# Kernel tuning notes

Hardware: AMD Instinct MI355X
Metric: run time of the kernel (lower is better)

Reference implementation:

```python
import jax, jax.numpy as jnp
import numpy as np

N = 50000      # nodes
F = 128        # in_channels
H = 4          # heads
C = 32         # out_channels per head
E = 800000     # edges (before self-loops)
NEG_SLOPE = 0.2


def setup_inputs() -> dict:
    key = jax.random.key(0)
    ks = jax.random.split(key, 10)
    x = jax.random.normal(ks[0], (N, F), dtype=jnp.float32)
    edge_index = jax.random.randint(ks[1], (2, E), 0, N, dtype=jnp.int32)
    s = 1.0 / np.sqrt(F)
    Wl = jax.random.uniform(ks[2], (H * C, F), jnp.float32, -s, s)
    bl = jax.random.uniform(ks[3], (H * C,), jnp.float32, -s, s)
    Wr = jax.random.uniform(ks[4], (H * C, F), jnp.float32, -s, s)
    br = jax.random.uniform(ks[5], (H * C,), jnp.float32, -s, s)
    Ws = jax.random.uniform(ks[6], (H * C, F), jnp.float32, -s, s)
    bs = jax.random.uniform(ks[7], (H * C,), jnp.float32, -s, s)
    att = jax.random.normal(ks[8], (H, C), jnp.float32) * (1.0 / np.sqrt(C))
    bias = jnp.zeros((H * C,), jnp.float32)
    return {"x": x, "edge_index": edge_index, "Wl": Wl, "bl": bl,
            "Wr": Wr, "br": br, "Ws": Ws, "bs": bs, "att": att, "bias": bias}


def reference(x, edge_index, Wl, bl, Wr, br, Ws, bs, att, bias):
    # add self loops (add_self_loops=True, edge_dim=None)
    loop = jnp.arange(N, dtype=edge_index.dtype)
    src = jnp.concatenate([edge_index[0], loop])  # j (source / neighbor)
    dst = jnp.concatenate([edge_index[1], loop])  # i (target, softmax segment)

    xl = (x @ Wl.T + bl).reshape(N, H, C)  # attention source transform (lin_l = lin_lAP)
    xr = (x @ Wr.T + br).reshape(N, H, C)  # attention target transform (lin_r = lin_rAP)
    xs = (x @ Ws.T + bs).reshape(N, H, C)  # aggregation transform (lin_s, linAggrSharing=False)

    # GATv2 edge score: a^T LeakyReLU(Theta_l x_j + Theta_r x_i)
    e = jax.nn.leaky_relu(xl[src] + xr[dst], NEG_SLOPE)      # [E+N, H, C]
    score = jnp.einsum('ehc,hc->eh', e, att)                 # [E+N, H]

    # segment softmax over incoming edges of each target node
    m = jax.ops.segment_max(score, dst, num_segments=N)      # [N, H]
    p = jnp.exp(score - m[dst])
    denom = jax.ops.segment_sum(p, dst, num_segments=N)      # [N, H]
    alpha = p / denom[dst]                                   # [E+N, H]

    # weighted scatter-add aggregation of lin_s-transformed sources
    out = jax.ops.segment_sum(xs[src] * alpha[..., None], dst, num_segments=N)
    return out.reshape(N, H * C) + bias                      # concat=True
```

## Files before the change

### kernel.cpp

```cpp
#include <hip/hip_runtime.h>
#include <hip/hip_bf16.h>

#define GN 50000
#define GF 128
#define GH 4
#define GC 32
#define GE 800000
#define GETOT (GE + GN)
#define HC 128
#define NEG 0.2f

#define TBLK ((GN + 63) / 64)
#define SBLK ((GETOT + 255) / 256)

typedef __bf16 bf16x8 __attribute__((ext_vector_type(8)));
typedef float  f32x4  __attribute__((ext_vector_type(4)));
typedef unsigned short ushort8 __attribute__((ext_vector_type(8)));

__device__ __forceinline__ ushort f32_to_bf16_rne(float f) {
    unsigned u = __float_as_uint(f);
    return (ushort)((u + 0x7fffu + ((u >> 16) & 1u)) >> 16);
}

__device__ __forceinline__ bf16x8 cvt8(const float* p) {
    float4 v0 = *(const float4*)p;
    float4 v1 = *(const float4*)(p + 4);
    ushort8 o;
    o[0] = f32_to_bf16_rne(v0.x); o[1] = f32_to_bf16_rne(v0.y);
    o[2] = f32_to_bf16_rne(v0.z); o[3] = f32_to_bf16_rne(v0.w);
    o[4] = f32_to_bf16_rne(v1.x); o[5] = f32_to_bf16_rne(v1.y);
    o[6] = f32_to_bf16_rne(v1.z); o[7] = f32_to_bf16_rne(v1.w);
    return __builtin_bit_cast(bf16x8, o);
}

template<int CTRL>
__device__ __forceinline__ float dpp_add(float v) {
    int s = __builtin_bit_cast(int, v);
    int y = __builtin_amdgcn_update_dpp(s, s, CTRL, 0xF, 0xF, false);
    return v + __builtin_bit_cast(float, y);
}

__global__ __launch_bounds__(256) void conv_w(
    const float* __restrict__ Wl, const float* __restrict__ Wr,
    const float* __restrict__ Ws, ushort* __restrict__ Wb,
    int* __restrict__ deg)
{
    int idx = blockIdx.x * 256 + threadIdx.x;
    if (idx < 3 * GF * GF / 8) {
        int m = idx / 2048;
        int e = (idx - m * 2048) * 8;
        const float* W = (m == 0) ? Wl : (m == 1) ? Wr : Ws;
        float4 v0 = *(const float4*)&W[e];
        float4 v1 = *(const float4*)&W[e + 4];
        ushort8 o;
        o[0] = f32_to_bf16_rne(v0.x); o[1] = f32_to_bf16_rne(v0.y);
        o[2] = f32_to_bf16_rne(v0.z); o[3] = f32_to_bf16_rne(v0.w);
        o[4] = f32_to_bf16_rne(v1.x); o[5] = f32_to_bf16_rne(v1.y);
        o[6] = f32_to_bf16_rne(v1.z); o[7] = f32_to_bf16_rne(v1.w);
        *(ushort8*)&Wb[m * 16384 + e] = o;
    }
    int z = idx - 6144;
    if (z >= 0 && z < GN / 4)
        *(int4*)&deg[z * 4] = make_int4(0, 0, 0, 0);
}

__global__ __launch_bounds__(256) void fused_transform_slot(
    const float* __restrict__ x, const ushort* __restrict__ Wb,
    const float* __restrict__ bl, const float* __restrict__ br,
    const float* __restrict__ bs,
    const int* __restrict__ ei, int* __restrict__ deg, int* __restrict__ slot,
    ushort* __restrict__ xi, float* __restrict__ xr)
{
    if (blockIdx.x < SBLK) {
        int e = blockIdx.x * 256 + threadIdx.x;
        if (e < GETOT) {
            int dst = (e < GE) ? ei[GE + e] : (e - GE);
            slot[e] = atomicAdd(&deg[dst], 1);
        }
        return;
    }

    const int bx    = blockIdx.x - SBLK;
    const int wave  = threadIdx.x >> 6;
    const int lane  = threadIdx.x & 63;
    const int colb  = lane & 15;
    const int klane = lane >> 4;
    const int row0  = bx * 64 + wave * 16;

    bf16x8 a[4];
    {
        int rA = row0 + colb;
        const float* ap = x + (size_t)min(rA, GN - 1) * GF + klane * 8;
#pragma unroll
        for (int kb = 0; kb < 4; ++kb)
            a[kb] = cvt8(ap + kb * 32);
    }

    for (int m = 0; m < 3; ++m) {
        const ushort* wb = Wb + m * 16384 + colb * GF + klane * 8;

        f32x4 acc[8];
#pragma unroll
        for (int n = 0; n < 8; ++n) acc[n] = (f32x4){0.f, 0.f, 0.f, 0.f};

#pragma unroll
        for (int kb = 0; kb < 4; ++kb) {
            bf16x8 b[8];
#pragma unroll
            for (int n = 0; n < 8; ++n)
                b[n] = *(const bf16x8*)(wb + n * 2048 + kb * 32);
#pragma unroll
            for (int n = 0; n < 8; ++n)
                acc[n] = __builtin_amdgcn_mfma_f32_16x16x32_bf16(a[kb], b[n], acc[n], 0, 0, 0);
        }

        const float* bia = (m == 0) ? bl : (m == 1) ? br : bs;
        const int moff = (m == 2) ? 2 : 0;
        const int rD0 = row0 + klane * 4;
#pragma unroll
        for (int n = 0; n < 8; ++n) {
            int col = n * 16 + colb;
            float bv = bia[col];
#pragma unroll
            for (int r = 0; r < 4; ++r) {
                int row = rD0 + r;
                if (row < GN) {
                    float v = acc[n][r] + bv;
                    if (m == 1)
                        xr[(size_t)row * HC + col] = v;
                    else
                        xi[(size_t)row * 256 + (col >> 1) * 4 + (col & 1) + moff]
                            = f32_to_bf16_rne(v);
                }
            }
        }
    }
}

__global__ __launch_bounds__(1024) void scan_kernel(const int* __restrict__ deg,
                                                    int* __restrict__ rowstart)
{
    __shared__ int sums[1024];
    const int t = threadIdx.x;
    const int CH = 52;
    const int start = t * CH;
    const int end = min(start + CH, GN);

    int s = 0;
    if (start + CH <= GN) {
#pragma unroll
        for (int g = 0; g < 13; ++g) {
            int4 v = *(const int4*)&deg[start + g * 4];
            s += v.x + v.y + v.z + v.w;
        }
    } else {
        for (int i = start; i < end; ++i) s += deg[i];
    }
    sums[t] = s;
    __syncthreads();
    for (int off = 1; off < 1024; off <<= 1) {
        int v = (t >= off) ? sums[t - off] : 0;
        __syncthreads();
        sums[t] += v;
        __syncthreads();
    }
    int run = sums[t] - s;
    if (start + CH <= GN) {
#pragma unroll
        for (int g = 0; g < 13; ++g) {
            int4 v = *(const int4*)&deg[start + g * 4];
            int4 w;
            w.x = run;
            w.y = run + v.x;
            w.z = run + v.x + v.y;
            w.w = run + v.x + v.y + v.z;
            run += v.x + v.y + v.z + v.w;
            *(int4*)&rowstart[start + g * 4] = w;
        }
    } else {
        for (int i = start; i < end; ++i) { rowstart[i] = run; run += deg[i]; }
    }
    if (t == 1023) rowstart[GN] = run;
}

__global__ void scatter_kernel(const int* __restrict__ ei,
                               const int* __restrict__ rowstart,
                               const int* __restrict__ slot,
                               int* __restrict__ csr_src)
{
    int e = blockIdx.x * 256 + threadIdx.x;
    if (e >= GETOT) return;
    int src, dst;
    if (e < GE) { src = ei[e]; dst = ei[GE + e]; }
    else        { src = dst = e - GE; }
    csr_src[rowstart[dst] + slot[e]] = src;
}

__device__ __forceinline__ void edge_acc(uint2 xv, float2 xr2, float2 at2,
                                         bool live, float& denom,
                                         float& ax, float& ay)
{
    float zx = __uint_as_float((xv.x & 0xffffu) << 16) + xr2.x;
    float zy = __uint_as_float(xv.x & 0xffff0000u) + xr2.y;
    zx = (zx > 0.f) ? zx : NEG * zx;
    zy = (zy > 0.f) ? zy : NEG * zy;
    float sc = fmaf(zx, at2.x, zy * at2.y);
    sc = dpp_add<0xB1>(sc);
    sc = dpp_add<0x4E>(sc);
    sc = dpp_add<0x124>(sc);
    sc = dpp_add<0x128>(sc);
    float pe = live ? __expf(sc) : 0.f;
    denom += pe;
    ax = fmaf(pe, __uint_as_float((xv.y & 0xffffu) << 16), ax);
    ay = fmaf(pe, __uint_as_float(xv.y & 0xffff0000u), ay);
}

__global__ __launch_bounds__(256) void gat_kernel(
    const ushort* __restrict__ xi, const float* __restrict__ xr,
    const float* __restrict__ att, const float* __restrict__ bias,
    const int* __restrict__ rowstart, const int* __restrict__ csr_src,
    float* __restrict__ out)
{
    const int wave = threadIdx.x >> 6;
    const int lane = threadIdx.x & 63;
    const int node = blockIdx.x * 4 + wave;
    const int l4 = lane * 4;

    const float2 xr2 = *(const float2*)&xr[(size_t)node * HC + lane * 2];
    const float2 at2 = *(const float2*)&att[lane * 2];
    const float2 bi2 = *(const float2*)&bias[lane * 2];

    const int s0 = rowstart[node];
    const int s1 = rowstart[node + 1];

    float denom = 0.f, ax = 0.f, ay = 0.f;
    for (int base = s0; base < s1; base += 64) {
        int nsrc = (base + lane < s1) ? csr_src[base + lane] : 0;
        int cnt = min(64, s1 - base);
        for (int t = 0; t < cnt; t += 4) {
            int sA = __shfl(nsrc, t, 64);
            int sB = __shfl(nsrc, t + 1, 64);
            int sC = __shfl(nsrc, t + 2, 64);
            int sD = __shfl(nsrc, t + 3, 64);
            uint2 vA = *(const uint2*)&xi[(size_t)sA * 256 + l4];
            uint2 vB = *(const uint2*)&xi[(size_t)sB * 256 + l4];
            uint2 vC = *(const uint2*)&xi[(size_t)sC * 256 + l4];
            uint2 vD = *(const uint2*)&xi[(size_t)sD * 256 + l4];
            edge_acc(vA, xr2, at2, true,          denom, ax, ay);
            edge_acc(vB, xr2, at2, (t + 1 < cnt), denom, ax, ay);
            edge_acc(vC, xr2, at2, (t + 2 < cnt), denom, ax, ay);
            edge_acc(vD, xr2, at2, (t + 3 < cnt), denom, ax, ay);
        }
    }
    const float inv = 1.f / denom;
    float2 o;
    o.x = fmaf(ax, inv, bi2.x);
    o.y = fmaf(ay, inv, bi2.y);
    *(float2*)&out[(size_t)node * HC + lane * 2] = o;
}

extern "C" void kernel_launch(void* const* d_in, const int* in_sizes, int n_in,
                              void* d_out, int out_size, void* d_ws, size_t ws_size,
                              hipStream_t stream)
{
    const float* x   = (const float*)d_in[0];
    const int*   ei  = (const int*)  d_in[1];
    const float* Wl  = (const float*)d_in[2];
    const float* bl  = (const float*)d_in[3];
    const float* Wr  = (const float*)d_in[4];
    const float* br  = (const float*)d_in[5];
    const float* Ws  = (const float*)d_in[6];
    const float* bs  = (const float*)d_in[7];
    const float* att = (const float*)d_in[8];
    const float* bias= (const float*)d_in[9];
    float* out = (float*)d_out;

    ushort* xi = (ushort*)d_ws;
    ushort* Wb = xi + (size_t)GN * 256;
    float*  xr = (float*)(Wb + 3 * GF * GF);
    int* deg      = (int*)(xr + (size_t)GN * HC);
    int* rowstart = deg + GN;
    int* slot     = rowstart + GN + 1;
    int* csr_src  = slot + GETOT;

    conv_w<<<(6144 + GN / 4 + 255) / 256, 256, 0, stream>>>(Wl, Wr, Ws, Wb, deg);

    fused_transform_slot<<<SBLK + TBLK, 256, 0, stream>>>(
        x, Wb, bl, br, bs, ei, deg, slot, xi, xr);

    scan_kernel<<<1, 1024, 0, stream>>>(deg, rowstart);

    scatter_kernel<<<SBLK, 256, 0, stream>>>(ei, rowstart, slot, csr_src);

    gat_kernel<<<GN / 4, 256, 0, stream>>>((const ushort*)xi, xr, att, bias,
                                           rowstart, csr_src, out);
}
```

Measured before the change: 285.9 us.

## Stage transform outputs through LDS for coalesced stores and pack xl/xs interleaved

The transform kernel now computes the Wl and Ws products together, packs their bf16 results pairwise into 32-bit words and stages them through shared memory, so each row is written with coalesced 16-byte stores. The xr output goes through the same LDS staging. The packed xi layout shrinks from 256 ushorts to 128 uints per row, and the gather kernel's unpacking is adjusted to match. Block order is also swapped so the transform blocks come before the slot-counting blocks. This aims to cut uncoalesced scattered 2-byte and 4-byte global stores, at the cost of about 33KB of LDS per block, which may lower occupancy.

Result: faster. 248.7 us (-13.0%).

```diff
diff --git a/kernel.cpp b/kernel.cpp
--- a/kernel.cpp
+++ b/kernel.cpp
@@ -12,24 +12,25 @@
 
 #define TBLK ((GN + 63) / 64)
 #define SBLK ((GETOT + 255) / 256)
+#define LDSW 132
 
 typedef __bf16 bf16x8 __attribute__((ext_vector_type(8)));
 typedef float  f32x4  __attribute__((ext_vector_type(4)));
 typedef unsigned short ushort8 __attribute__((ext_vector_type(8)));
 
-__device__ __forceinline__ ushort f32_to_bf16_rne(float f) {
+__device__ __forceinline__ uint f32_to_bf16_rne(float f) {
     unsigned u = __float_as_uint(f);
-    return (ushort)((u + 0x7fffu + ((u >> 16) & 1u)) >> 16);
+    return (u + 0x7fffu + ((u >> 16) & 1u)) >> 16;
 }
 
 __device__ __forceinline__ bf16x8 cvt8(const float* p) {
     float4 v0 = *(const float4*)p;
     float4 v1 = *(const float4*)(p + 4);
     ushort8 o;
-    o[0] = f32_to_bf16_rne(v0.x); o[1] = f32_to_bf16_rne(v0.y);
-    o[2] = f32_to_bf16_rne(v0.z); o[3] = f32_to_bf16_rne(v0.w);
-    o[4] = f32_to_bf16_rne(v1.x); o[5] = f32_to_bf16_rne(v1.y);
-    o[6] = f32_to_bf16_rne(v1.z); o[7] = f32_to_bf16_rne(v1.w);
+    o[0] = (ushort)f32_to_bf16_rne(v0.x); o[1] = (ushort)f32_to_bf16_rne(v0.y);
+    o[2] = (ushort)f32_to_bf16_rne(v0.z); o[3] = (ushort)f32_to_bf16_rne(v0.w);
+    o[4] = (ushort)f32_to_bf16_rne(v1.x); o[5] = (ushort)f32_to_bf16_rne(v1.y);
+    o[6] = (ushort)f32_to_bf16_rne(v1.z); o[7] = (ushort)f32_to_bf16_rne(v1.w);
     return __builtin_bit_cast(bf16x8, o);
 }
 
@@ -53,10 +54,10 @@
         float4 v0 = *(const float4*)&W[e];
         float4 v1 = *(const float4*)&W[e + 4];
         ushort8 o;
-        o[0] = f32_to_bf16_rne(v0.x); o[1] = f32_to_bf16_rne(v0.y);
-        o[2] = f32_to_bf16_rne(v0.z); o[3] = f32_to_bf16_rne(v0.w);
-        o[4] = f32_to_bf16_rne(v1.x); o[5] = f32_to_bf16_rne(v1.y);
-        o[6] = f32_to_bf16_rne(v1.z); o[7] = f32_to_bf16_rne(v1.w);
+        o[0] = (ushort)f32_to_bf16_rne(v0.x); o[1] = (ushort)f32_to_bf16_rne(v0.y);
+        o[2] = (ushort)f32_to_bf16_rne(v0.z); o[3] = (ushort)f32_to_bf16_rne(v0.w);
+        o[4] = (ushort)f32_to_bf16_rne(v1.x); o[5] = (ushort)f32_to_bf16_rne(v1.y);
+        o[6] = (ushort)f32_to_bf16_rne(v1.z); o[7] = (ushort)f32_to_bf16_rne(v1.w);
         *(ushort8*)&Wb[m * 16384 + e] = o;
     }
     int z = idx - 6144;
@@ -69,10 +70,12 @@
     const float* __restrict__ bl, const float* __restrict__ br,
     const float* __restrict__ bs,
     const int* __restrict__ ei, int* __restrict__ deg, int* __restrict__ slot,
-    ushort* __restrict__ xi, float* __restrict__ xr)
-{
-    if (blockIdx.x < SBLK) {
-        int e = blockIdx.x * 256 + threadIdx.x;
+    uint* __restrict__ xi, float* __restrict__ xr)
+{
+    __shared__ float lds_f[64 * LDSW];
+
+    if (blockIdx.x >= TBLK) {
+        int e = (blockIdx.x - TBLK) * 256 + threadIdx.x;
         if (e < GETOT) {
             int dst = (e < GE) ? ei[GE + e] : (e - GE);
             slot[e] = atomicAdd(&deg[dst], 1);
@@ -80,9 +83,10 @@
         return;
     }
 
-    const int bx    = blockIdx.x - SBLK;
-    const int wave  = threadIdx.x >> 6;
-    const int lane  = threadIdx.x & 63;
+    const int bx    = blockIdx.x;
+    const int tid   = threadIdx.x;
+    const int wave  = tid >> 6;
+    const int lane  = tid & 63;
     const int colb  = lane & 15;
     const int klane = lane >> 4;
     const int row0  = bx * 64 + wave * 16;
@@ -96,43 +100,81 @@
             a[kb] = cvt8(ap + kb * 32);
     }
 
-    for (int m = 0; m < 3; ++m) {
-        const ushort* wb = Wb + m * 16384 + colb * GF + klane * 8;
-
-        f32x4 acc[8];
-#pragma unroll
-        for (int n = 0; n < 8; ++n) acc[n] = (f32x4){0.f, 0.f, 0.f, 0.f};
-
-#pragma unroll
-        for (int kb = 0; kb < 4; ++kb) {
-            bf16x8 b[8];
-#pragma unroll
-            for (int n = 0; n < 8; ++n)
-                b[n] = *(const bf16x8*)(wb + n * 2048 + kb * 32);
-#pragma unroll
-            for (int n = 0; n < 8; ++n)
-                acc[n] = __builtin_amdgcn_mfma_f32_16x16x32_bf16(a[kb], b[n], acc[n], 0, 0, 0);
-        }
-
-        const float* bia = (m == 0) ? bl : (m == 1) ? br : bs;
-        const int moff = (m == 2) ? 2 : 0;
-        const int rD0 = row0 + klane * 4;
+    const int woff = colb * GF + klane * 8;
+    uint* lds_u = (uint*)lds_f;
+
+    f32x4 acc0[8], acc2[8];
+#pragma unroll
+    for (int n = 0; n < 8; ++n) {
+        acc0[n] = (f32x4){0.f, 0.f, 0.f, 0.f};
+        acc2[n] = (f32x4){0.f, 0.f, 0.f, 0.f};
+    }
+#pragma unroll
+    for (int kb = 0; kb < 4; ++kb) {
+        const ushort* w0 = Wb + woff + kb * 32;
+        const ushort* w2 = Wb + 2 * 16384 + woff + kb * 32;
 #pragma unroll
         for (int n = 0; n < 8; ++n) {
-            int col = n * 16 + colb;
-            float bv = bia[col];
-#pragma unroll
-            for (int r = 0; r < 4; ++r) {
-                int row = rD0 + r;
-                if (row < GN) {
-                    float v = acc[n][r] + bv;
-                    if (m == 1)
-                        xr[(size_t)row * HC + col] = v;
-                    else
-                        xi[(size_t)row * 256 + (col >> 1) * 4 + (col & 1) + moff]
-                            = f32_to_bf16_rne(v);
-                }
-            }
+            bf16x8 b0 = *(const bf16x8*)(w0 + n * 2048);
+            bf16x8 b2 = *(const bf16x8*)(w2 + n * 2048);
+            acc0[n] = __builtin_amdgcn_mfma_f32_16x16x32_bf16(a[kb], b0, acc0[n], 0, 0, 0);
+            acc2[n] = __builtin_amdgcn_mfma_f32_16x16x32_bf16(a[kb], b2, acc2[n], 0, 0, 0);
+        }
+    }
+#pragma unroll
+    for (int n = 0; n < 8; ++n) {
+        int col = n * 16 + colb;
+        float blv = bl[col], bsv = bs[col];
+#pragma unroll
+        for (int r = 0; r < 4; ++r) {
+            int rl = wave * 16 + klane * 4 + r;
+            uint w = f32_to_bf16_rne(acc0[n][r] + blv)
+                   | (f32_to_bf16_rne(acc2[n][r] + bsv) << 16);
+            lds_u[rl * LDSW + col] = w;
+        }
+    }
+    __syncthreads();
+#pragma unroll
+    for (int i = 0; i < 8; ++i) {
+        int c = i * 256 + tid;
+        int row = c >> 5, cin = c & 31;
+        if (bx * 64 + row < GN) {
+            uint4 v = *(uint4*)&lds_u[row * LDSW + cin * 4];
+            *(uint4*)&xi[((size_t)(bx * 64 + row)) * 128 + cin * 4] = v;
+        }
+    }
+    __syncthreads();
+
+    f32x4 acc1[8];
+#pragma unroll
+    for (int n = 0; n < 8; ++n) acc1[n] = (f32x4){0.f, 0.f, 0.f, 0.f};
+#pragma unroll
+    for (int kb = 0; kb < 4; ++kb) {
+        const ushort* w1 = Wb + 16384 + woff + kb * 32;
+#pragma unroll
+        for (int n = 0; n < 8; ++n) {
+            bf16x8 b1 = *(const bf16x8*)(w1 + n * 2048);
+            acc1[n] = __builtin_amdgcn_mfma_f32_16x16x32_bf16(a[kb], b1, acc1[n], 0, 0, 0);
+        }
+    }
+#pragma unroll
+    for (int n = 0; n < 8; ++n) {
+        int col = n * 16 + colb;
+        float bv = br[col];
+#pragma unroll
+        for (int r = 0; r < 4; ++r) {
+            int rl = wave * 16 + klane * 4 + r;
+            lds_f[rl * LDSW + col] = acc1[n][r] + bv;
+        }
+    }
+    __syncthreads();
+#pragma unroll
+    for (int i = 0; i < 8; ++i) {
+        int c = i * 256 + tid;
+        int row = c >> 5, cin = c & 31;
+        if (bx * 64 + row < GN) {
+            float4 v = *(float4*)&lds_f[row * LDSW + cin * 4];
+            *(float4*)&xr[((size_t)(bx * 64 + row)) * 128 + cin * 4] = v;
         }
     }
 }
@@ -201,7 +243,7 @@
                                          float& ax, float& ay)
 {
     float zx = __uint_as_float((xv.x & 0xffffu) << 16) + xr2.x;
-    float zy = __uint_as_float(xv.x & 0xffff0000u) + xr2.y;
+    float zy = __uint_as_float((xv.y & 0xffffu) << 16) + xr2.y;
     zx = (zx > 0.f) ? zx : NEG * zx;
     zy = (zy > 0.f) ? zy : NEG * zy;
     float sc = fmaf(zx, at2.x, zy * at2.y);
@@ -211,12 +253,12 @@
     sc = dpp_add<0x128>(sc);
     float pe = live ? __expf(sc) : 0.f;
     denom += pe;
-    ax = fmaf(pe, __uint_as_float((xv.y & 0xffffu) << 16), ax);
+    ax = fmaf(pe, __uint_as_float(xv.x & 0xffff0000u), ax);
     ay = fmaf(pe, __uint_as_float(xv.y & 0xffff0000u), ay);
 }
 
 __global__ __launch_bounds__(256) void gat_kernel(
-    const ushort* __restrict__ xi, const float* __restrict__ xr,
+    const uint* __restrict__ xi, const float* __restrict__ xr,
     const float* __restrict__ att, const float* __restrict__ bias,
     const int* __restrict__ rowstart, const int* __restrict__ csr_src,
     float* __restrict__ out)
@@ -224,11 +266,11 @@
     const int wave = threadIdx.x >> 6;
     const int lane = threadIdx.x & 63;
     const int node = blockIdx.x * 4 + wave;
-    const int l4 = lane * 4;
-
-    const float2 xr2 = *(const float2*)&xr[(size_t)node * HC + lane * 2];
-    const float2 at2 = *(const float2*)&att[lane * 2];
-    const float2 bi2 = *(const float2*)&bias[lane * 2];
+    const int l2 = lane * 2;
+
+    const float2 xr2 = *(const float2*)&xr[(size_t)node * HC + l2];
+    const float2 at2 = *(const float2*)&att[l2];
+    const float2 bi2 = *(const float2*)&bias[l2];
 
     const int s0 = rowstart[node];
     const int s1 = rowstart[node + 1];
@@ -242,10 +284,10 @@
             int sB = __shfl(nsrc, t + 1, 64);
             int sC = __shfl(nsrc, t + 2, 64);
             int sD = __shfl(nsrc, t + 3, 64);
-            uint2 vA = *(const uint2*)&xi[(size_t)sA * 256 + l4];
-            uint2 vB = *(const uint2*)&xi[(size_t)sB * 256 + l4];
-            uint2 vC = *(const uint2*)&xi[(size_t)sC * 256 + l4];
-            uint2 vD = *(const uint2*)&xi[(size_t)sD * 256 + l4];
+            uint2 vA = *(const uint2*)&xi[(size_t)sA * 128 + l2];
+            uint2 vB = *(const uint2*)&xi[(size_t)sB * 128 + l2];
+            uint2 vC = *(const uint2*)&xi[(size_t)sC * 128 + l2];
+            uint2 vD = *(const uint2*)&xi[(size_t)sD * 128 + l2];
             edge_acc(vA, xr2, at2, true,          denom, ax, ay);
             edge_acc(vB, xr2, at2, (t + 1 < cnt), denom, ax, ay);
             edge_acc(vC, xr2, at2, (t + 2 < cnt), denom, ax, ay);
@@ -256,7 +298,7 @@
     float2 o;
     o.x = fmaf(ax, inv, bi2.x);
     o.y = fmaf(ay, inv, bi2.y);
-    *(float2*)&out[(size_t)node * HC + lane * 2] = o;
+    *(float2*)&out[(size_t)node * HC + l2] = o;
 }
 
 extern "C" void kernel_launch(void* const* d_in, const int* in_sizes, int n_in,
@@ -275,8 +317,8 @@
     const float* bias= (const float*)d_in[9];
     float* out = (float*)d_out;
 
-    ushort* xi = (ushort*)d_ws;
-    ushort* Wb = xi + (size_t)GN * 256;
+    uint*   xi = (uint*)d_ws;
+    ushort* Wb = (ushort*)(xi + (size_t)GN * 128);
     float*  xr = (float*)(Wb + 3 * GF * GF);
     int* deg      = (int*)(xr + (size_t)GN * HC);
     int* rowstart = deg + GN;
@@ -285,13 +327,13 @@
 
     conv_w<<<(6144 + GN / 4 + 255) / 256, 256, 0, stream>>>(Wl, Wr, Ws, Wb, deg);
 
-    fused_transform_slot<<<SBLK + TBLK, 256, 0, stream>>>(
+    fused_transform_slot<<<TBLK + SBLK, 256, 0, stream>>>(
         x, Wb, bl, br, bs, ei, deg, slot, xi, xr);
 
     scan_kernel<<<1, 1024, 0, stream>>>(deg, rowstart);
 
     scatter_kernel<<<SBLK, 256, 0, stream>>>(ei, rowstart, slot, csr_src);
 
-    gat_kernel<<<GN / 4, 256, 0, stream>>>((const ushort*)xi, xr, att, bias,
+    gat_kernel<<<GN / 4, 256, 0, stream>>>((const uint*)xi, xr, att, bias,
                                            rowstart, csr_src, out);
 }
```
